# Kernel tuning notes

Measured on AMD Instinct MI355X. Metric: run time of the kernel, lower is better.

## Reference

```python
import jax, jax.numpy as jnp
import numpy as np
from math import sqrt

D_MODEL = 1024
N_HEADS = 16
FFN = 4096
B, N = 2, 2048
EPS = 1e-5


def _layernorm(x, g, b):
    mu = jnp.mean(x, -1, keepdims=True)
    var = jnp.mean((x - mu) ** 2, -1, keepdims=True)
    return (x - mu) * jax.lax.rsqrt(var + EPS) * g + b


def setup_inputs() -> dict:
    key = jax.random.key(0)
    ks = jax.random.split(key, 12)
    s = 1.0 / sqrt(D_MODEL)
    sf = 1.0 / sqrt(FFN)
    inp = {
        "tgt": jax.random.normal(ks[0], (B, N, D_MODEL), jnp.float32),
        # True = masked. Causal: query i may attend to keys j <= i.
        "tgt_mask": jnp.triu(jnp.ones((N, N), jnp.bool_), k=1),
        "tgt_key_pad_mask": jnp.zeros((B, N), jnp.bool_),
        "Wq": jax.random.uniform(ks[1], (D_MODEL, D_MODEL), jnp.float32, -s, s),
        "Wk": jax.random.uniform(ks[2], (D_MODEL, D_MODEL), jnp.float32, -s, s),
        "Wv": jax.random.uniform(ks[3], (D_MODEL, D_MODEL), jnp.float32, -s, s),
        "Wo": jax.random.uniform(ks[4], (D_MODEL, D_MODEL), jnp.float32, -s, s),
        "bo": jax.random.uniform(ks[5], (D_MODEL,), jnp.float32, -s, s),
        "W1": jax.random.uniform(ks[6], (FFN, D_MODEL), jnp.float32, -s, s),
        "b1": jax.random.uniform(ks[7], (FFN,), jnp.float32, -s, s),
        "W2": jax.random.uniform(ks[8], (D_MODEL, FFN), jnp.float32, -sf, sf),
        "b2": jax.random.uniform(ks[9], (D_MODEL,), jnp.float32, -sf, sf),
        "g1": jnp.ones((D_MODEL,), jnp.float32),
        "beta1": jnp.zeros((D_MODEL,), jnp.float32),
        "g2": jnp.ones((D_MODEL,), jnp.float32),
        "beta2": jnp.zeros((D_MODEL,), jnp.float32),
    }
    return inp


def _mha(x, tgt_mask, pad_mask, Wq, Wk, Wv, Wo, bo):
    b, n, d = x.shape
    dk = d // N_HEADS
    q = (x @ Wq.T).reshape(b, n, N_HEADS, dk).transpose(0, 2, 1, 3)  # bhnd
    k = (x @ Wk.T).reshape(b, n, N_HEADS, dk).transpose(0, 2, 1, 3)
    v = (x @ Wv.T).reshape(b, n, N_HEADS, dk).transpose(0, 2, 1, 3)
    scores = jnp.einsum("bhqd,bhkd->bhqk", q, k) / sqrt(dk)
    mask = tgt_mask[None, None, :, :] | pad_mask[:, None, None, :]
    scores = jnp.where(mask, -jnp.inf, scores)
    att = jax.nn.softmax(scores, axis=-1)
    out = jnp.einsum("bhqk,bhkd->bhqd", att, v).transpose(0, 2, 1, 3).reshape(b, n, d)
    return out @ Wo.T + bo


def reference(tgt, tgt_mask, tgt_key_pad_mask, Wq, Wk, Wv, Wo, bo,
              W1, b1, W2, b2, g1, beta1, g2, beta2):
    # PostNorm logic (pre_norm=False), dropout=0 (eval)
    h = _mha(tgt, tgt_mask, tgt_key_pad_mask, Wq, Wk, Wv, Wo, bo)
    x = _layernorm(tgt + h, g1, beta1)
    m = jax.nn.gelu(x @ W1.T + b1, approximate=True) @ W2.T + b2
    return _layernorm(x + m, g2, beta2)
```

## Files before the change

### kernel.cpp

```cpp
#include <hip/hip_runtime.h>


#define DEV __device__ __forceinline__

typedef __attribute__((ext_vector_type(4)))  float f32x4;
typedef __attribute__((ext_vector_type(16))) float f32x16;
typedef __attribute__((ext_vector_type(8)))  short s16x8;

static constexpr int Bb   = 2;
static constexpr int NN   = 2048;
static constexpr int DM   = 1024;
static constexpr int HH   = 16;
static constexpr int DK   = 64;
static constexpr int FF   = 4096;
static constexpr int ROWS = Bb * NN;

#define AS1(p) ((const __attribute__((address_space(1))) void*)(p))
#define AS3(p) ((__attribute__((address_space(3))) void*)(p))

DEV unsigned short f2bf(float f) {
  unsigned u = __float_as_uint(f);
  u += 0x7fff + ((u >> 16) & 1);
  return (unsigned short)(u >> 16);
}
DEV float fexp2(float x) {
  float r;
  asm("v_exp_f32 %0, %1" : "=v"(r) : "v"(x));
  return r;
}
DEV unsigned cvtpk(float lo, float hi) {
  unsigned r;
  asm("v_cvt_pk_bf16_f32 %0, %1, %2" : "=v"(r) : "v"(lo), "v"(hi));
  return r;
}

__global__ __launch_bounds__(256) void k_cast7(
    const float* __restrict__ tgt, const float* __restrict__ Wq,
    const float* __restrict__ Wk, const float* __restrict__ Wv,
    const float* __restrict__ Wo, const float* __restrict__ W1,
    const float* __restrict__ W2,
    ushort* __restrict__ xb, ushort* __restrict__ wqb,
    ushort* __restrict__ w1b, ushort* __restrict__ w2b) {
  const int i = blockIdx.x * 256 + threadIdx.x;
  constexpr int S0 = 1048576;
  constexpr int S1 = 262144;
  const float4* src;
  ushort* dstp;
  if (i < S0)               { src = (const float4*)tgt + i;            dstp = xb  + (size_t)i * 4; }
  else if (i < S0 + S1)     { src = (const float4*)Wq + (i - S0);      dstp = wqb + (size_t)(i - S0) * 4; }
  else if (i < S0 + 2 * S1) { src = (const float4*)Wk + (i - S0 - S1); dstp = wqb + (size_t)(i - S0) * 4; }
  else if (i < S0 + 3 * S1) { src = (const float4*)Wv + (i - S0 - 2 * S1); dstp = wqb + (size_t)(i - S0) * 4; }
  else if (i < S0 + 4 * S1) { src = (const float4*)Wo + (i - S0 - 3 * S1); dstp = wqb + (size_t)(i - S0) * 4; }
  else if (i < 3 * S0)      { src = (const float4*)W1 + (i - 2 * S0);  dstp = w1b + (size_t)(i - 2 * S0) * 4; }
  else                      { src = (const float4*)W2 + (i - 3 * S0);  dstp = w2b + (size_t)(i - 3 * S0) * 4; }
  float4 v = *src;
  ushort4 o;
  o.x = f2bf(v.x); o.y = f2bf(v.y); o.z = f2bf(v.z); o.w = f2bf(v.w);
  *reinterpret_cast<ushort4*>(dstp) = o;
}

template <int EPI, int BN, bool QKV, int SPLITK>
__global__ __launch_bounds__(256) void k_gemm(
    const ushort* __restrict__ A, const ushort* __restrict__ Bt,
    const float* __restrict__ bias, const float* __restrict__ resid,
    ushort* __restrict__ Cb, float* __restrict__ Cf,
    int K, int nbx) {
  __shared__ ushort As[3][128][32];
  __shared__ ushort Bs[3][BN][32];

  const int t = threadIdx.x;
  const int lane = t & 63, w = t >> 6;
  const int lr = lane & 15, lg = lane >> 4;
  const int lrow = lane >> 2, lc8 = (lane & 3) * 8;

  const int nwg = gridDim.x;
  const int bid = blockIdx.x;
  const int q8 = nwg >> 3, r8 = nwg & 7;
  const int xcd = bid & 7, lin = bid >> 3;
  int wg = (xcd < r8 ? xcd * (q8 + 1) : r8 * (q8 + 1) + (xcd - r8) * q8) + lin;
  int kc = 0;
  if constexpr (SPLITK == 2) { kc = wg & 1; wg >>= 1; }
  const int band = wg / (4 * nbx);
  const int inn  = wg % (4 * nbx);
  const int by = band * 4 + (inn & 3);
  const int bx = inn >> 2;

  const int bRow = by * 128;
  const int bCol = bx * BN;
  const int Kc = K / SPLITK;
  const int kofs = kc * Kc;
  const int nk = Kc / 32;

  constexpr int NW = BN / 32;
  const int wRow = (w >> 1) * 64, wCol = (w & 1) * (BN / 2);

  const f32x4 zero = {0.f, 0.f, 0.f, 0.f};
  f32x4 acc[4][NW];
#pragma unroll
  for (int m = 0; m < 4; ++m)
#pragma unroll
    for (int n = 0; n < NW; ++n) acc[m][n] = zero;

  auto stage = [&](int buf, int tile) {
    const int kb = kofs + tile * 32;
#pragma unroll
    for (int i = 0; i < 2; ++i) {
      int rr = w * 32 + i * 16;
      __builtin_amdgcn_global_load_lds(
          AS1(A + (size_t)(bRow + rr + lrow) * K + kb + lc8),
          AS3(&As[buf][rr][0]), 16, 0, 0);
    }
#pragma unroll
    for (int i = 0; i < BN / 64; ++i) {
      int rr = w * (BN / 4) + i * 16;
      __builtin_amdgcn_global_load_lds(
          AS1(Bt + (size_t)(bCol + rr + lrow) * K + kb + lc8),
          AS3(&Bs[buf][rr][0]), 16, 0, 0);
    }
  };

  stage(0, 0);
  stage(1, 1);
  for (int tt = 0; tt < nk; ++tt) {
    const int cur = tt % 3;
    if (tt + 2 < nk) {
      stage((tt + 2) % 3, tt + 2);
      if constexpr (BN == 128) asm volatile("s_waitcnt vmcnt(8)" ::: "memory");
      else                     asm volatile("s_waitcnt vmcnt(6)" ::: "memory");
    } else if (tt + 1 < nk) {
      if constexpr (BN == 128) asm volatile("s_waitcnt vmcnt(4)" ::: "memory");
      else                     asm volatile("s_waitcnt vmcnt(3)" ::: "memory");
    } else {
      asm volatile("s_waitcnt vmcnt(0)" ::: "memory");
    }
    __builtin_amdgcn_s_barrier();
    __builtin_amdgcn_sched_barrier(0);

    s16x8 af[4], bfr[NW];
#pragma unroll
    for (int m = 0; m < 4; ++m)
      af[m] = *reinterpret_cast<const s16x8*>(&As[cur][wRow + m * 16 + lr][lg * 8]);
#pragma unroll
    for (int n = 0; n < NW; ++n)
      bfr[n] = *reinterpret_cast<const s16x8*>(&Bs[cur][wCol + n * 16 + lr][lg * 8]);
#pragma unroll
    for (int m = 0; m < 4; ++m)
#pragma unroll
      for (int n = 0; n < NW; ++n)
        acc[m][n] = __builtin_amdgcn_mfma_f32_16x16x32_bf16(af[m], bfr[n], acc[m][n], 0, 0, 0);

    asm volatile("s_waitcnt lgkmcnt(0)" ::: "memory");
    __builtin_amdgcn_s_barrier();
    __builtin_amdgcn_sched_barrier(0);
  }

  ushort* CbOut = Cb;
  int colBase = bCol, Ncols = nbx * BN, third = 0;
  if (QKV) {
    third = bCol >> 10;
    CbOut = Cb + (size_t)third * ROWS * DM;
    colBase = bCol & 1023;
    Ncols = DM;
  }
#pragma unroll
  for (int m = 0; m < 4; ++m) {
    int gr = bRow + wRow + m * 16 + lg * 4;
#pragma unroll
    for (int n = 0; n < NW; ++n) {
      int gc = colBase + wCol + n * 16 + lr;
      float bv = (EPI == 1 || EPI == 2) ? bias[gc] : 0.0f;
#pragma unroll
      for (int r = 0; r < 4; ++r) {
        int nr = gr + r;
        float v = acc[m][n][r] + bv;
        if (EPI == 3) {
          Cf[((size_t)kc * ROWS + nr) * Ncols + gc] = v;
        } else if (EPI == 2) {
          size_t idx = (size_t)nr * Ncols + gc;
          Cf[idx] = v + resid[idx];
        } else if (EPI == 1) {
          size_t idx = (size_t)nr * Ncols + gc;
          float u = v + 0.044715f * v * v * v;
          float g = v / (1.0f + __expf(-1.5957691216057308f * u));
          CbOut[idx] = f2bf(g);
        } else {
          int gcs = gc;
          if (QKV && third == 1)
            gcs = (gc & ~63) | ((gc ^ ((nr & 7) << 3)) & 63);
          CbOut[(size_t)nr * Ncols + gcs] = f2bf(v);
        }
      }
    }
  }
}

__global__ __launch_bounds__(256) void k_vt(const ushort* __restrict__ V,
                                            ushort* __restrict__ vT) {
  __shared__ ushort Ls[64][72];
  const int t = threadIdx.x;
  const int n0 = blockIdx.x * 64;
  const int bh = blockIdx.y;
  const int b = bh >> 4, h = bh & 15;
  const int n = t >> 2;
#pragma unroll
  for (int half = 0; half < 2; ++half) {
    int c8 = ((t & 3) + half * 4) * 8;
    int4 v = *reinterpret_cast<const int4*>(
        V + ((size_t)(b * NN + n0 + n)) * DM + h * DK + c8);
    *reinterpret_cast<int4*>(&Ls[n][c8]) = v;
  }
  __syncthreads();
  const int d = t >> 2;
#pragma unroll
  for (int half = 0; half < 2; ++half) {
    int c = (t & 3) + half * 4;
    ushort tmp[8];
#pragma unroll
    for (int j = 0; j < 8; ++j) tmp[j] = Ls[c * 8 + j][d];
    size_t out = ((size_t)bh * DK + d) * NN + n0 + ((c ^ (d & 7)) * 8);
    *reinterpret_cast<int4*>(vT + out) = *reinterpret_cast<const int4*>(tmp);
  }
}

template <int WB, int RED>
__global__ __launch_bounds__(256) void k_ln(const float* __restrict__ in,
                                            const float* __restrict__ p0,
                                            const float* __restrict__ p1,
                                            const float* __restrict__ pb,
                                            const float* __restrict__ g,
                                            const float* __restrict__ bta,
                                            float* __restrict__ outf,
                                            ushort* __restrict__ outb) {
  const int row = blockIdx.x;
  const int t = threadIdx.x;
  float4 v = reinterpret_cast<const float4*>(in + (size_t)row * DM)[t];
  if (RED) {
    float4 a = reinterpret_cast<const float4*>(p0 + (size_t)row * DM)[t];
    float4 b = reinterpret_cast<const float4*>(p1 + (size_t)row * DM)[t];
    float4 c = reinterpret_cast<const float4*>(pb)[t];
    v.x += a.x + b.x + c.x;
    v.y += a.y + b.y + c.y;
    v.z += a.z + b.z + c.z;
    v.w += a.w + b.w + c.w;
  }
  float s1 = v.x + v.y + v.z + v.w;
  float s2 = v.x * v.x + v.y * v.y + v.z * v.z + v.w * v.w;
#pragma unroll
  for (int m = 32; m; m >>= 1) {
    s1 += __shfl_xor(s1, m, 64);
    s2 += __shfl_xor(s2, m, 64);
  }
  __shared__ float red[2][4];
  if ((t & 63) == 0) { red[0][t >> 6] = s1; red[1][t >> 6] = s2; }
  __syncthreads();
  s1 = red[0][0] + red[0][1] + red[0][2] + red[0][3];
  s2 = red[1][0] + red[1][1] + red[1][2] + red[1][3];
  const float mu = s1 * (1.0f / DM);
  const float var = s2 * (1.0f / DM) - mu * mu;
  const float rstd = rsqrtf(var + 1e-5f);
  float4 gv = reinterpret_cast<const float4*>(g)[t];
  float4 bv = reinterpret_cast<const float4*>(bta)[t];
  float4 o;
  o.x = (v.x - mu) * rstd * gv.x + bv.x;
  o.y = (v.y - mu) * rstd * gv.y + bv.y;
  o.z = (v.z - mu) * rstd * gv.z + bv.z;
  o.w = (v.w - mu) * rstd * gv.w + bv.w;
  reinterpret_cast<float4*>(outf + (size_t)row * DM)[t] = o;
  if (WB) {
    ushort4 ob;
    ob.x = f2bf(o.x); ob.y = f2bf(o.y); ob.z = f2bf(o.z); ob.w = f2bf(o.w);
    reinterpret_cast<ushort4*>(outb + (size_t)row * DM)[t] = ob;
  }
}

static __device__ const unsigned char SCHED24[24][2] = {
  {15,0},{15,1},{7,2},
  {14,0},{14,1},{13,0},{13,1},{6,2},
  {12,0},{12,1},{11,0},{11,1},{5,2},
  {10,0},{10,1},{9,0},{9,1},{4,2},
  {8,0},{8,1},{3,2},{2,2},{1,2},{0,2}};

__global__ __launch_bounds__(256) void k_attn(const ushort* __restrict__ Q,
                                              const ushort* __restrict__ Kb,
                                              const ushort* __restrict__ vT,
                                              ushort* __restrict__ O,
                                              float* __restrict__ Op,
                                              float* __restrict__ ml) {
  __shared__ ushort Ks[2][64 * 64];
  __shared__ ushort Vs[2][64 * 64];

  const int t = threadIdx.x;
  const int bid = blockIdx.x;
  const int xcd = bid & 7, j = bid >> 3;
  const int head = j / 24, e = j % 24;
  const int qi = SCHED24[e][0], sv = SCHED24[e][1];
  const int bh = xcd * 4 + head;
  const int kt0 = (sv == 1) ? (qi + 1) : 0;
  const int kt1 = (sv == 0) ? (qi + 1) : (2 * qi + 2);

  const int lane = t & 63, wid = t >> 6;
  const int l31 = lane & 31, hi = lane >> 5;
  const int q0w = qi * 128 + wid * 32;
  const size_t qbase = ((size_t)(bh >> 4) * NN) * DM + (bh & 15) * DK;
  const size_t vbase = (size_t)bh * DK * NN;

  const float C = 0.18033688011112043f;

  s16x8 qf[4];
#pragma unroll
  for (int c = 0; c < 4; ++c)
    qf[c] = *reinterpret_cast<const s16x8*>(Q + qbase + (size_t)(q0w + l31) * DM + c * 16 + hi * 8);

  float mrun = -1e30f, lrun = 0.f, negcm = 1e30f;
  f32x16 accO[2];
#pragma unroll
  for (int dt = 0; dt < 2; ++dt)
#pragma unroll
    for (int r = 0; r < 16; ++r) accO[dt][r] = 0.f;

  auto stage = [&](int buf, int kt) {
    const int kk = kt * 64;
#pragma unroll
    for (int i = 0; i < 2; ++i) {
      int row0 = wid * 16 + i * 8;
      __builtin_amdgcn_global_load_lds(
          AS1(Kb + qbase + (size_t)(kk + row0 + (lane >> 3)) * DM + (lane & 7) * 8),
          AS3(&Ks[buf][row0 * 64]), 16, 0, 0);
      __builtin_amdgcn_global_load_lds(
          AS1(vT + vbase + (size_t)(row0 + (lane >> 3)) * NN + kk + (lane & 7) * 8),
          AS3(&Vs[buf][row0 * 64]), 16, 0, 0);
    }
  };

  stage(0, kt0);
  for (int kt = kt0, li = 0; kt < kt1; ++kt, ++li) {
    const int cur = li & 1;
    const int kk = kt * 64;
    __syncthreads();
    if (kt + 1 < kt1) stage(cur ^ 1, kt + 1);

    if (kk <= q0w + 31) {
      const char* KsB = (const char*)Ks[cur];
      const char* VsB = (const char*)Vs[cur];
      const bool diag = (kk + 64 > q0w);
      const int nsub = (kk + 32 <= q0w + 31) ? 2 : 1;

      f32x16 st[2];
      __builtin_amdgcn_s_setprio(1);
#pragma unroll
      for (int sub = 0; sub < 2; ++sub) {
        if (sub >= nsub) break;
#pragma unroll
        for (int r = 0; r < 16; ++r) st[sub][r] = 0.f;
        const int row = sub * 32 + l31;
        const int swz = (row & 7) << 4;
#pragma unroll
        for (int c = 0; c < 4; ++c) {
          s16x8 kf = *reinterpret_cast<const s16x8*>(KsB + row * 128 + ((c * 32 + hi * 16) ^ swz));
          st[sub] = __builtin_amdgcn_mfma_f32_32x32x16_bf16(kf, qf[c], st[sub], 0, 0, 0);
        }
      }
      __builtin_amdgcn_s_setprio(0);

      const int q = q0w + l31;
      float p[32];
#pragma unroll
      for (int sub = 0; sub < 2; ++sub) {
        if (sub >= nsub) break;
#pragma unroll
        for (int r = 0; r < 16; ++r) {
          float v = st[sub][r];
          if (diag) {
            int kl = sub * 32 + (r & 3) + 8 * (r >> 2) + 4 * hi;
            if (kk + kl > q) v = -1e30f;
          }
          p[sub * 16 + r] = v;
        }
      }
      float a[16];
#pragma unroll
      for (int i = 0; i < 16; ++i) a[i] = (nsub == 2) ? fmaxf(p[i], p[i + 16]) : p[i];
#pragma unroll
      for (int s = 8; s; s >>= 1)
#pragma unroll
        for (int i = 0; i < 8; ++i) if (i < s) a[i] = fmaxf(a[i], a[i + s]);
      float rm = fmaxf(a[0], __shfl_xor(a[0], 32, 64));

      if (__any(rm > mrun)) {
        const float mn = fmaxf(mrun, rm);
        const float alpha = fexp2(C * (mrun - mn));
        mrun = mn;
        negcm = -C * mn;
        lrun *= alpha;
#pragma unroll
        for (int dt = 0; dt < 2; ++dt) accO[dt] *= alpha;
      }

#pragma unroll
      for (int sub = 0; sub < 2; ++sub) {
        if (sub >= nsub) break;
#pragma unroll
        for (int i = 0; i < 16; ++i)
          p[sub * 16 + i] = fexp2(fmaf(p[sub * 16 + i], C, negcm));
      }
#pragma unroll
      for (int i = 0; i < 16; ++i) a[i] = (nsub == 2) ? (p[i] + p[i + 16]) : p[i];
#pragma unroll
      for (int s = 8; s; s >>= 1)
#pragma unroll
        for (int i = 0; i < 8; ++i) if (i < s) a[i] += a[i + s];
      lrun += a[0] + __shfl_xor(a[0], 32, 64);

      s16x8 pf[4];
#pragma unroll
      for (int sub = 0; sub < 2; ++sub) {
        if (sub >= nsub) break;
#pragma unroll
        for (int hf = 0; hf < 2; ++hf) {
          const float* pp = &p[sub * 16 + hf * 8];
          unsigned X0 = cvtpk(pp[0], pp[1]);
          unsigned X1 = cvtpk(pp[2], pp[3]);
          unsigned Y0 = cvtpk(pp[4], pp[5]);
          unsigned Y1 = cvtpk(pp[6], pp[7]);
          asm volatile("v_permlane32_swap_b32 %0, %1" : "+v"(X0), "+v"(Y0));
          asm volatile("v_permlane32_swap_b32 %0, %1" : "+v"(X1), "+v"(Y1));
          union { unsigned u[4]; s16x8 v; } uu;
          uu.u[0] = X0; uu.u[1] = X1; uu.u[2] = Y0; uu.u[3] = Y1;
          pf[sub * 2 + hf] = uu.v;
        }
      }

      __builtin_amdgcn_s_setprio(1);
#pragma unroll
      for (int dt = 0; dt < 2; ++dt) {
        const int d = dt * 32 + l31;
        const int vswz = (d & 7) << 4;
#pragma unroll
        for (int kc = 0; kc < 4; ++kc) {
          if (kc >= nsub * 2) break;
          s16x8 vf = *reinterpret_cast<const s16x8*>(VsB + d * 128 + ((kc * 32 + hi * 16) ^ vswz));
          accO[dt] = __builtin_amdgcn_mfma_f32_32x32x16_bf16(vf, pf[kc], accO[dt], 0, 0, 0);
        }
      }
      __builtin_amdgcn_s_setprio(0);
    }
  }

  if (sv == 2) {
    const int q = q0w + l31;
    const float inv = 1.0f / lrun;
#pragma unroll
    for (int dt = 0; dt < 2; ++dt)
#pragma unroll
      for (int rg = 0; rg < 4; ++rg) {
        int d0 = 8 * rg + 4 * hi + 32 * dt;
        ushort4 ov;
        ov.x = f2bf(accO[dt][rg * 4 + 0] * inv);
        ov.y = f2bf(accO[dt][rg * 4 + 1] * inv);
        ov.z = f2bf(accO[dt][rg * 4 + 2] * inv);
        ov.w = f2bf(accO[dt][rg * 4 + 3] * inv);
        *reinterpret_cast<ushort4*>(O + qbase + (size_t)q * DM + d0) = ov;
      }
  } else {
    const int pidx = (bh * 8 + (qi - 8)) * 2 + sv;
    float* op = Op + (size_t)pidx * (128 * 64);
    const int row = wid * 32 + l31;
#pragma unroll
    for (int dt = 0; dt < 2; ++dt)
#pragma unroll
      for (int rg = 0; rg < 4; ++rg) {
        int d0 = 8 * rg + 4 * hi + 32 * dt;
        f32x4 v4 = { accO[dt][rg * 4 + 0], accO[dt][rg * 4 + 1],
                     accO[dt][rg * 4 + 2], accO[dt][rg * 4 + 3] };
        *reinterpret_cast<f32x4*>(op + (size_t)row * 64 + d0) = v4;
      }
    if (hi == 0) {
      ml[(size_t)pidx * 256 + row * 2 + 0] = mrun;
      ml[(size_t)pidx * 256 + row * 2 + 1] = lrun;
    }
  }
}

__global__ __launch_bounds__(256) void k_amerge(const float* __restrict__ Op,
                                                const float* __restrict__ ml,
                                                ushort* __restrict__ O) {
  const int bh = blockIdx.x >> 3, qq = blockIdx.x & 7;
  const int t = threadIdx.x;
  const int row = t >> 1, dh = (t & 1) * 32;
  const float C = 0.18033688011112043f;

  const int p0 = (bh * 8 + qq) * 2;
  const float m0 = ml[(size_t)p0 * 256 + row * 2 + 0];
  const float l0 = ml[(size_t)p0 * 256 + row * 2 + 1];
  const float m1 = ml[(size_t)(p0 + 1) * 256 + row * 2 + 0];
  const float l1 = ml[(size_t)(p0 + 1) * 256 + row * 2 + 1];
  const float M = fmaxf(m0, m1);
  const float s0 = fexp2(C * (m0 - M));
  const float s1 = fexp2(C * (m1 - M));
  const float inv = 1.0f / (l0 * s0 + l1 * s1);

  const float* o0 = Op + (size_t)p0 * (128 * 64) + (size_t)row * 64 + dh;
  const float* o1 = o0 + 128 * 64;
  const int b = bh >> 4, h = bh & 15;
  const int n = (qq + 8) * 128 + row;
  ushort* dst = O + ((size_t)(b * NN + n)) * DM + h * DK + dh;
#pragma unroll
  for (int i = 0; i < 8; ++i) {
    float4 a = reinterpret_cast<const float4*>(o0)[i];
    float4 c = reinterpret_cast<const float4*>(o1)[i];
    ushort4 ov;
    ov.x = f2bf((a.x * s0 + c.x * s1) * inv);
    ov.y = f2bf((a.y * s0 + c.y * s1) * inv);
    ov.z = f2bf((a.z * s0 + c.z * s1) * inv);
    ov.w = f2bf((a.w * s0 + c.w * s1) * inv);
    reinterpret_cast<ushort4*>(dst)[i] = ov;
  }
}

extern "C" void kernel_launch(void* const* d_in, const int* in_sizes, int n_in,
                              void* d_out, int out_size, void* d_ws, size_t ws_size,
                              hipStream_t stream) {
  const float* tgt = (const float*)d_in[0];
  const float* Wq  = (const float*)d_in[3];
  const float* Wk  = (const float*)d_in[4];
  const float* Wv  = (const float*)d_in[5];
  const float* Wo  = (const float*)d_in[6];
  const float* bo  = (const float*)d_in[7];
  const float* W1  = (const float*)d_in[8];
  const float* b1  = (const float*)d_in[9];
  const float* W2  = (const float*)d_in[10];
  const float* b2  = (const float*)d_in[11];
  const float* g1  = (const float*)d_in[12];
  const float* be1 = (const float*)d_in[13];
  const float* g2  = (const float*)d_in[14];
  const float* be2 = (const float*)d_in[15];

  char* ws = (char*)d_ws;
  size_t off = 0;
  auto alloc = [&](size_t bytes) {
    void* p = ws + off;
    off += (bytes + 255) & ~(size_t)255;
    return p;
  };
  ushort* xb   = (ushort*)alloc((size_t)ROWS * DM * 2);
  ushort* wqb  = (ushort*)alloc((size_t)DM * DM * 2);
  ushort* wkb  = (ushort*)alloc((size_t)DM * DM * 2);
  ushort* wvb  = (ushort*)alloc((size_t)DM * DM * 2);
  ushort* wob  = (ushort*)alloc((size_t)DM * DM * 2);
  ushort* w1b  = (ushort*)alloc((size_t)FF * DM * 2);
  ushort* w2b  = (ushort*)alloc((size_t)DM * FF * 2);
  ushort* qbuf = (ushort*)alloc((size_t)ROWS * DM * 2);
  ushort* kbuf = (ushort*)alloc((size_t)ROWS * DM * 2);
  ushort* vbuf = (ushort*)alloc((size_t)ROWS * DM * 2);
  ushort* vtb  = (ushort*)alloc((size_t)ROWS * DM * 2);
  ushort* atnb = (ushort*)alloc((size_t)ROWS * DM * 2);
  float*  h1   = (float*)alloc((size_t)ROWS * DM * 4);
  float*  x1f  = (float*)alloc((size_t)ROWS * DM * 4);
  ushort* x1b  = (ushort*)alloc((size_t)ROWS * DM * 2);
  ushort* t1b  = (ushort*)alloc((size_t)ROWS * FF * 2);
  float*  Opb  = (float*)alloc((size_t)512 * 128 * 64 * 4);
  float*  mlb  = (float*)alloc((size_t)512 * 256 * 4);
  float*  pp   = (float*)qbuf;
  (void)ws_size; (void)in_sizes; (void)n_in; (void)out_size;
  (void)wkb; (void)wvb; (void)kbuf;

  dim3 blk(256);
  k_cast7<<<dim3(16384), blk, 0, stream>>>(tgt, Wq, Wk, Wv, Wo, W1, W2,
                                           xb, wqb, w1b, w2b);

  k_gemm<0, 128, true, 1><<<dim3(24 * 32), blk, 0, stream>>>(
      xb, wqb, nullptr, nullptr, qbuf, nullptr, DM, 24);

  k_vt<<<dim3(NN / 64, Bb * HH), blk, 0, stream>>>(vbuf, vtb);

  k_attn<<<dim3(768), blk, 0, stream>>>(qbuf, kbuf, vtb, atnb, Opb, mlb);
  k_amerge<<<dim3(256), blk, 0, stream>>>(Opb, mlb, atnb);

  k_gemm<2, 64, false, 1><<<dim3(16 * 32), blk, 0, stream>>>(
      atnb, wob, bo, tgt, nullptr, h1, DM, 16);
  k_ln<1, 0><<<dim3(ROWS), blk, 0, stream>>>(h1, nullptr, nullptr, nullptr,
                                             g1, be1, x1f, x1b);

  k_gemm<1, 128, false, 1><<<dim3(32 * 32), blk, 0, stream>>>(
      x1b, w1b, b1, nullptr, t1b, nullptr, DM, 32);
  k_gemm<3, 64, false, 2><<<dim3(2 * 16 * 32), blk, 0, stream>>>(
      t1b, w2b, nullptr, nullptr, nullptr, pp, FF, 16);
  k_ln<0, 1><<<dim3(ROWS), blk, 0, stream>>>(x1f, pp, pp + (size_t)ROWS * DM, b2,
                                             g2, be2, (float*)d_out, nullptr);
}
```

Baseline: 272.2 us.

## Load attention K/V fragments directly from global into registers, dropping LDS staging

The attention kernel no longer stages K and V tiles through shared memory with global_load_lds and block barriers. Each wave now loads its MFMA operand fragments straight from global memory into registers, double-buffering K fragments across iterations and capping the tile loop at the wave's causal limit. The XOR swizzles on K and vT written by the QKV GEMM epilogue and the transpose kernel are removed to match. This removes barrier synchronisation and LDS traffic, but each wave re-reads K/V that its four waves used to share, which adds global/L2 traffic and register pressure.

```diff
diff --git a/kernel.cpp b/kernel.cpp
--- a/kernel.cpp
+++ b/kernel.cpp
@@ -155,10 +155,9 @@
   }
 
   ushort* CbOut = Cb;
-  int colBase = bCol, Ncols = nbx * BN, third = 0;
+  int colBase = bCol, Ncols = nbx * BN;
   if (QKV) {
-    third = bCol >> 10;
-    CbOut = Cb + (size_t)third * ROWS * DM;
+    CbOut = Cb + (size_t)(bCol >> 10) * ROWS * DM;
     colBase = bCol & 1023;
     Ncols = DM;
   }
@@ -184,10 +183,7 @@
           float g = v / (1.0f + __expf(-1.5957691216057308f * u));
           CbOut[idx] = f2bf(g);
         } else {
-          int gcs = gc;
-          if (QKV && third == 1)
-            gcs = (gc & ~63) | ((gc ^ ((nr & 7) << 3)) & 63);
-          CbOut[(size_t)nr * Ncols + gcs] = f2bf(v);
+          CbOut[(size_t)nr * Ncols + gc] = f2bf(v);
         }
       }
     }
@@ -217,7 +213,7 @@
     ushort tmp[8];
 #pragma unroll
     for (int j = 0; j < 8; ++j) tmp[j] = Ls[c * 8 + j][d];
-    size_t out = ((size_t)bh * DK + d) * NN + n0 + ((c ^ (d & 7)) * 8);
+    size_t out = ((size_t)bh * DK + d) * NN + n0 + c * 8;
     *reinterpret_cast<int4*>(vT + out) = *reinterpret_cast<const int4*>(tmp);
   }
 }
@@ -286,9 +282,6 @@
                                               ushort* __restrict__ O,
                                               float* __restrict__ Op,
                                               float* __restrict__ ml) {
-  __shared__ ushort Ks[2][64 * 64];
-  __shared__ ushort Vs[2][64 * 64];
-
   const int t = threadIdx.x;
   const int bid = blockIdx.x;
   const int xcd = bid & 7, j = bid >> 3;
@@ -303,8 +296,10 @@
   const int q0w = qi * 128 + wid * 32;
   const size_t qbase = ((size_t)(bh >> 4) * NN) * DM + (bh & 15) * DK;
   const size_t vbase = (size_t)bh * DK * NN;
-
   const float C = 0.18033688011112043f;
+
+  const int ktcap = ((q0w + 31) >> 6) + 1;
+  const int ktend = (kt1 < ktcap) ? kt1 : ktcap;
 
   s16x8 qf[4];
 #pragma unroll
@@ -318,132 +313,138 @@
 #pragma unroll
     for (int r = 0; r < 16; ++r) accO[dt][r] = 0.f;
 
-  auto stage = [&](int buf, int kt) {
+  const ushort* kRow = Kb + qbase + (size_t)l31 * DM + hi * 8;
+  const ushort* vRow = vT + vbase + (size_t)l31 * NN + hi * 8;
+
+  s16x8 kfA[8], kfB[8], vf[8];
+
+  auto loadK = [&](s16x8* kf, int kt) {
+#pragma unroll
+    for (int sub = 0; sub < 2; ++sub)
+#pragma unroll
+      for (int c = 0; c < 4; ++c)
+        kf[sub * 4 + c] = *reinterpret_cast<const s16x8*>(
+            kRow + (size_t)(kt * 64 + sub * 32) * DM + c * 16);
+  };
+  auto loadV = [&](int kt) {
+#pragma unroll
+    for (int dt = 0; dt < 2; ++dt)
+#pragma unroll
+      for (int kc = 0; kc < 4; ++kc)
+        vf[dt * 4 + kc] = *reinterpret_cast<const s16x8*>(
+            vRow + (size_t)(dt * 32) * NN + kt * 64 + kc * 16);
+  };
+
+  auto tilecomp = [&](const s16x8* kf, int kt) {
     const int kk = kt * 64;
-#pragma unroll
-    for (int i = 0; i < 2; ++i) {
-      int row0 = wid * 16 + i * 8;
-      __builtin_amdgcn_global_load_lds(
-          AS1(Kb + qbase + (size_t)(kk + row0 + (lane >> 3)) * DM + (lane & 7) * 8),
-          AS3(&Ks[buf][row0 * 64]), 16, 0, 0);
-      __builtin_amdgcn_global_load_lds(
-          AS1(vT + vbase + (size_t)(row0 + (lane >> 3)) * NN + kk + (lane & 7) * 8),
-          AS3(&Vs[buf][row0 * 64]), 16, 0, 0);
-    }
+    const bool diag = (kk + 64 > q0w);
+    const int nsub = (kk + 32 <= q0w + 31) ? 2 : 1;
+
+    f32x16 st[2];
+    __builtin_amdgcn_s_setprio(1);
+#pragma unroll
+    for (int sub = 0; sub < 2; ++sub) {
+      if (sub >= nsub) break;
+#pragma unroll
+      for (int r = 0; r < 16; ++r) st[sub][r] = 0.f;
+#pragma unroll
+      for (int c = 0; c < 4; ++c)
+        st[sub] = __builtin_amdgcn_mfma_f32_32x32x16_bf16(kf[sub * 4 + c], qf[c], st[sub], 0, 0, 0);
+    }
+    __builtin_amdgcn_s_setprio(0);
+
+    const int q = q0w + l31;
+    float p[32];
+#pragma unroll
+    for (int sub = 0; sub < 2; ++sub) {
+      if (sub >= nsub) break;
+#pragma unroll
+      for (int r = 0; r < 16; ++r) {
+        float v = st[sub][r];
+        if (diag) {
+          int kl = sub * 32 + (r & 3) + 8 * (r >> 2) + 4 * hi;
+          if (kk + kl > q) v = -1e30f;
+        }
+        p[sub * 16 + r] = v;
+      }
+    }
+    float a[16];
+#pragma unroll
+    for (int i = 0; i < 16; ++i) a[i] = (nsub == 2) ? fmaxf(p[i], p[i + 16]) : p[i];
+#pragma unroll
+    for (int s = 8; s; s >>= 1)
+#pragma unroll
+      for (int i = 0; i < 8; ++i) if (i < s) a[i] = fmaxf(a[i], a[i + s]);
+    float rm = fmaxf(a[0], __shfl_xor(a[0], 32, 64));
+
+    if (__any(rm > mrun)) {
+      const float mn = fmaxf(mrun, rm);
+      const float alpha = fexp2(C * (mrun - mn));
+      mrun = mn;
+      negcm = -C * mn;
+      lrun *= alpha;
+#pragma unroll
+      for (int dt = 0; dt < 2; ++dt) accO[dt] *= alpha;
+    }
+
+#pragma unroll
+    for (int sub = 0; sub < 2; ++sub) {
+      if (sub >= nsub) break;
+#pragma unroll
+      for (int i = 0; i < 16; ++i)
+        p[sub * 16 + i] = fexp2(fmaf(p[sub * 16 + i], C, negcm));
+    }
+#pragma unroll
+    for (int i = 0; i < 16; ++i) a[i] = (nsub == 2) ? (p[i] + p[i + 16]) : p[i];
+#pragma unroll
+    for (int s = 8; s; s >>= 1)
+#pragma unroll
+      for (int i = 0; i < 8; ++i) if (i < s) a[i] += a[i + s];
+    lrun += a[0] + __shfl_xor(a[0], 32, 64);
+
+    s16x8 pf[4];
+#pragma unroll
+    for (int sub = 0; sub < 2; ++sub) {
+      if (sub >= nsub) break;
+#pragma unroll
+      for (int hf = 0; hf < 2; ++hf) {
+        const float* pp = &p[sub * 16 + hf * 8];
+        unsigned X0 = cvtpk(pp[0], pp[1]);
+        unsigned X1 = cvtpk(pp[2], pp[3]);
+        unsigned Y0 = cvtpk(pp[4], pp[5]);
+        unsigned Y1 = cvtpk(pp[6], pp[7]);
+        asm volatile("v_permlane32_swap_b32 %0, %1" : "+v"(X0), "+v"(Y0));
+        asm volatile("v_permlane32_swap_b32 %0, %1" : "+v"(X1), "+v"(Y1));
+        union { unsigned u[4]; s16x8 v; } uu;
+        uu.u[0] = X0; uu.u[1] = X1; uu.u[2] = Y0; uu.u[3] = Y1;
+        pf[sub * 2 + hf] = uu.v;
+      }
+    }
+
+    __builtin_amdgcn_s_setprio(1);
+#pragma unroll
+    for (int dt = 0; dt < 2; ++dt) {
+#pragma unroll
+      for (int kc = 0; kc < 4; ++kc) {
+        if (kc >= nsub * 2) break;
+        accO[dt] = __builtin_amdgcn_mfma_f32_32x32x16_bf16(vf[dt * 4 + kc], pf[kc], accO[dt], 0, 0, 0);
+      }
+    }
+    __builtin_amdgcn_s_setprio(0);
   };
 
-  stage(0, kt0);
-  for (int kt = kt0, li = 0; kt < kt1; ++kt, ++li) {
-    const int cur = li & 1;
-    const int kk = kt * 64;
-    __syncthreads();
-    if (kt + 1 < kt1) stage(cur ^ 1, kt + 1);
-
-    if (kk <= q0w + 31) {
-      const char* KsB = (const char*)Ks[cur];
-      const char* VsB = (const char*)Vs[cur];
-      const bool diag = (kk + 64 > q0w);
-      const int nsub = (kk + 32 <= q0w + 31) ? 2 : 1;
-
-      f32x16 st[2];
-      __builtin_amdgcn_s_setprio(1);
-#pragma unroll
-      for (int sub = 0; sub < 2; ++sub) {
-        if (sub >= nsub) break;
-#pragma unroll
-        for (int r = 0; r < 16; ++r) st[sub][r] = 0.f;
-        const int row = sub * 32 + l31;
-        const int swz = (row & 7) << 4;
-#pragma unroll
-        for (int c = 0; c < 4; ++c) {
-          s16x8 kf = *reinterpret_cast<const s16x8*>(KsB + row * 128 + ((c * 32 + hi * 16) ^ swz));
-          st[sub] = __builtin_amdgcn_mfma_f32_32x32x16_bf16(kf, qf[c], st[sub], 0, 0, 0);
-        }
-      }
-      __builtin_amdgcn_s_setprio(0);
-
-      const int q = q0w + l31;
-      float p[32];
-#pragma unroll
-      for (int sub = 0; sub < 2; ++sub) {
-        if (sub >= nsub) break;
-#pragma unroll
-        for (int r = 0; r < 16; ++r) {
-          float v = st[sub][r];
-          if (diag) {
-            int kl = sub * 32 + (r & 3) + 8 * (r >> 2) + 4 * hi;
-            if (kk + kl > q) v = -1e30f;
-          }
-          p[sub * 16 + r] = v;
-        }
-      }
-      float a[16];
-#pragma unroll
-      for (int i = 0; i < 16; ++i) a[i] = (nsub == 2) ? fmaxf(p[i], p[i + 16]) : p[i];
-#pragma unroll
-      for (int s = 8; s; s >>= 1)
-#pragma unroll
-        for (int i = 0; i < 8; ++i) if (i < s) a[i] = fmaxf(a[i], a[i + s]);
-      float rm = fmaxf(a[0], __shfl_xor(a[0], 32, 64));
-
-      if (__any(rm > mrun)) {
-        const float mn = fmaxf(mrun, rm);
-        const float alpha = fexp2(C * (mrun - mn));
-        mrun = mn;
-        negcm = -C * mn;
-        lrun *= alpha;
-#pragma unroll
-        for (int dt = 0; dt < 2; ++dt) accO[dt] *= alpha;
-      }
-
-#pragma unroll
-      for (int sub = 0; sub < 2; ++sub) {
-        if (sub >= nsub) break;
-#pragma unroll
-        for (int i = 0; i < 16; ++i)
-          p[sub * 16 + i] = fexp2(fmaf(p[sub * 16 + i], C, negcm));
-      }
-#pragma unroll
-      for (int i = 0; i < 16; ++i) a[i] = (nsub == 2) ? (p[i] + p[i + 16]) : p[i];
-#pragma unroll
-      for (int s = 8; s; s >>= 1)
-#pragma unroll
-        for (int i = 0; i < 8; ++i) if (i < s) a[i] += a[i + s];
-      lrun += a[0] + __shfl_xor(a[0], 32, 64);
-
-      s16x8 pf[4];
-#pragma unroll
-      for (int sub = 0; sub < 2; ++sub) {
-        if (sub >= nsub) break;
-#pragma unroll
-        for (int hf = 0; hf < 2; ++hf) {
-          const float* pp = &p[sub * 16 + hf * 8];
-          unsigned X0 = cvtpk(pp[0], pp[1]);
-          unsigned X1 = cvtpk(pp[2], pp[3]);
-          unsigned Y0 = cvtpk(pp[4], pp[5]);
-          unsigned Y1 = cvtpk(pp[6], pp[7]);
-          asm volatile("v_permlane32_swap_b32 %0, %1" : "+v"(X0), "+v"(Y0));
-          asm volatile("v_permlane32_swap_b32 %0, %1" : "+v"(X1), "+v"(Y1));
-          union { unsigned u[4]; s16x8 v; } uu;
-          uu.u[0] = X0; uu.u[1] = X1; uu.u[2] = Y0; uu.u[3] = Y1;
-          pf[sub * 2 + hf] = uu.v;
-        }
-      }
-
-      __builtin_amdgcn_s_setprio(1);
-#pragma unroll
-      for (int dt = 0; dt < 2; ++dt) {
-        const int d = dt * 32 + l31;
-        const int vswz = (d & 7) << 4;
-#pragma unroll
-        for (int kc = 0; kc < 4; ++kc) {
-          if (kc >= nsub * 2) break;
-          s16x8 vf = *reinterpret_cast<const s16x8*>(VsB + d * 128 + ((kc * 32 + hi * 16) ^ vswz));
-          accO[dt] = __builtin_amdgcn_mfma_f32_32x32x16_bf16(vf, pf[kc], accO[dt], 0, 0, 0);
-        }
-      }
-      __builtin_amdgcn_s_setprio(0);
-    }
+  int kt = kt0;
+  if (kt < ktend) loadK(kfA, kt);
+  while (kt < ktend) {
+    loadV(kt);
+    if (kt + 1 < ktend) loadK(kfB, kt + 1);
+    tilecomp(kfA, kt);
+    ++kt;
+    if (kt >= ktend) break;
+    loadV(kt);
+    if (kt + 1 < ktend) loadK(kfA, kt + 1);
+    tilecomp(kfB, kt);
+    ++kt;
   }
 
   if (sv == 2) {
```

Result: slower. 291.9 us (+7.2%).

## Split causal attention KV into up to four segments with generalized merge

Applied to the files above, without the earlier changes.

Replaces the fixed 24-entry split-KV schedule with a 40-entry schedule where long query tiles are split into up to four KV segments (for qi>=4), and generalizes the merge kernel to combine a variable number of partials. The partial output buffer now aliases the h1 activation buffer instead of a dedicated allocation. This aims to balance per-block work across CUs, at the cost of more partial traffic and merge work, and relies on the aliased region (spilling past h1) being dead at that point.

```diff
diff --git a/kernel.cpp b/kernel.cpp
--- a/kernel.cpp
+++ b/kernel.cpp
@@ -273,12 +273,13 @@
   }
 }
 
-static __device__ const unsigned char SCHED24[24][2] = {
-  {15,0},{15,1},{7,2},
-  {14,0},{14,1},{13,0},{13,1},{6,2},
-  {12,0},{12,1},{11,0},{11,1},{5,2},
-  {10,0},{10,1},{9,0},{9,1},{4,2},
-  {8,0},{8,1},{3,2},{2,2},{1,2},{0,2}};
+static __device__ const unsigned char SCHED40[40][2] = {
+  {15,0},{15,1},{15,2},{15,3}, {14,0},{14,1},{14,2},{14,3},
+  {13,0},{13,1},{13,2},{13,3}, {12,0},{12,1},{12,2},{12,3},
+  {11,0},{11,1},{11,2}, {10,0},{10,1},{10,2},
+  {9,0},{9,1},{9,2}, {8,0},{8,1},{8,2},
+  {7,0},{7,1}, {6,0},{6,1}, {5,0},{5,1}, {4,0},{4,1},
+  {3,0},{2,0},{1,0},{0,0}};
 
 __global__ __launch_bounds__(256) void k_attn(const ushort* __restrict__ Q,
                                               const ushort* __restrict__ Kb,
@@ -292,11 +293,14 @@
   const int t = threadIdx.x;
   const int bid = blockIdx.x;
   const int xcd = bid & 7, j = bid >> 3;
-  const int head = j / 24, e = j % 24;
-  const int qi = SCHED24[e][0], sv = SCHED24[e][1];
+  const int head = j & 3, e = j >> 2;
+  const int qi = SCHED40[e][0], seg = SCHED40[e][1];
   const int bh = xcd * 4 + head;
-  const int kt0 = (sv == 1) ? (qi + 1) : 0;
-  const int kt1 = (sv == 0) ? (qi + 1) : (2 * qi + 2);
+  const int ntiles = 2 * qi + 2;
+  const int nseg = (2 * qi + 9) >> 3;
+  const int tb = ntiles / nseg, rem = ntiles % nseg;
+  const int kt0 = seg * tb + (seg < rem ? seg : rem);
+  const int kt1 = kt0 + tb + (seg < rem ? 1 : 0);
 
   const int lane = t & 63, wid = t >> 6;
   const int l31 = lane & 31, hi = lane >> 5;
@@ -446,7 +450,7 @@
     }
   }
 
-  if (sv == 2) {
+  if (nseg == 1) {
     const int q = q0w + l31;
     const float inv = 1.0f / lrun;
 #pragma unroll
@@ -462,7 +466,7 @@
         *reinterpret_cast<ushort4*>(O + qbase + (size_t)q * DM + d0) = ov;
       }
   } else {
-    const int pidx = (bh * 8 + (qi - 8)) * 2 + sv;
+    const int pidx = (bh * 12 + (qi - 4)) * 4 + seg;
     float* op = Op + (size_t)pidx * (128 * 64);
     const int row = wid * 32 + l31;
 #pragma unroll
@@ -484,35 +488,49 @@
 __global__ __launch_bounds__(256) void k_amerge(const float* __restrict__ Op,
                                                 const float* __restrict__ ml,
                                                 ushort* __restrict__ O) {
-  const int bh = blockIdx.x >> 3, qq = blockIdx.x & 7;
+  const int bid = blockIdx.x;
+  const int bh = bid / 12, qq = bid % 12;
+  const int qi = qq + 4;
+  const int nseg = (2 * qi + 9) >> 3;
   const int t = threadIdx.x;
   const int row = t >> 1, dh = (t & 1) * 32;
   const float C = 0.18033688011112043f;
-
-  const int p0 = (bh * 8 + qq) * 2;
-  const float m0 = ml[(size_t)p0 * 256 + row * 2 + 0];
-  const float l0 = ml[(size_t)p0 * 256 + row * 2 + 1];
-  const float m1 = ml[(size_t)(p0 + 1) * 256 + row * 2 + 0];
-  const float l1 = ml[(size_t)(p0 + 1) * 256 + row * 2 + 1];
-  const float M = fmaxf(m0, m1);
-  const float s0 = fexp2(C * (m0 - M));
-  const float s1 = fexp2(C * (m1 - M));
-  const float inv = 1.0f / (l0 * s0 + l1 * s1);
-
-  const float* o0 = Op + (size_t)p0 * (128 * 64) + (size_t)row * 64 + dh;
-  const float* o1 = o0 + 128 * 64;
+  const int pbase = (bh * 12 + qq) * 4;
+
+  float M = -1e30f;
+  for (int s = 0; s < nseg; ++s)
+    M = fmaxf(M, ml[(size_t)(pbase + s) * 256 + row * 2 + 0]);
+  float wsum = 0.f;
+  for (int s = 0; s < nseg; ++s) {
+    float ms = ml[(size_t)(pbase + s) * 256 + row * 2 + 0];
+    float ls = ml[(size_t)(pbase + s) * 256 + row * 2 + 1];
+    wsum += ls * fexp2(C * (ms - M));
+  }
+  const float inv = 1.0f / wsum;
+
+  f32x4 acc[8];
+#pragma unroll
+  for (int i = 0; i < 8; ++i) acc[i] = (f32x4){0.f, 0.f, 0.f, 0.f};
+  for (int s = 0; s < nseg; ++s) {
+    float ws = fexp2(C * (ml[(size_t)(pbase + s) * 256 + row * 2 + 0] - M));
+    const float* os = Op + (size_t)(pbase + s) * (128 * 64) + (size_t)row * 64 + dh;
+#pragma unroll
+    for (int i = 0; i < 8; ++i) {
+      f32x4 v = reinterpret_cast<const f32x4*>(os)[i];
+      acc[i] += v * ws;
+    }
+  }
+
   const int b = bh >> 4, h = bh & 15;
-  const int n = (qq + 8) * 128 + row;
+  const int n = qi * 128 + row;
   ushort* dst = O + ((size_t)(b * NN + n)) * DM + h * DK + dh;
 #pragma unroll
   for (int i = 0; i < 8; ++i) {
-    float4 a = reinterpret_cast<const float4*>(o0)[i];
-    float4 c = reinterpret_cast<const float4*>(o1)[i];
     ushort4 ov;
-    ov.x = f2bf((a.x * s0 + c.x * s1) * inv);
-    ov.y = f2bf((a.y * s0 + c.y * s1) * inv);
-    ov.z = f2bf((a.z * s0 + c.z * s1) * inv);
-    ov.w = f2bf((a.w * s0 + c.w * s1) * inv);
+    ov.x = f2bf(acc[i][0] * inv);
+    ov.y = f2bf(acc[i][1] * inv);
+    ov.z = f2bf(acc[i][2] * inv);
+    ov.w = f2bf(acc[i][3] * inv);
     reinterpret_cast<ushort4*>(dst)[i] = ov;
   }
 }
@@ -558,8 +576,8 @@
   float*  x1f  = (float*)alloc((size_t)ROWS * DM * 4);
   ushort* x1b  = (ushort*)alloc((size_t)ROWS * DM * 2);
   ushort* t1b  = (ushort*)alloc((size_t)ROWS * FF * 2);
-  float*  Opb  = (float*)alloc((size_t)512 * 128 * 64 * 4);
-  float*  mlb  = (float*)alloc((size_t)512 * 256 * 4);
+  float*  mlb  = (float*)alloc((size_t)1536 * 256 * 4);
+  float*  Opb  = h1;
   float*  pp   = (float*)qbuf;
   (void)ws_size; (void)in_sizes; (void)n_in; (void)out_size;
   (void)wkb; (void)wvb; (void)kbuf;
@@ -573,8 +591,8 @@
 
   k_vt<<<dim3(NN / 64, Bb * HH), blk, 0, stream>>>(vbuf, vtb);
 
-  k_attn<<<dim3(768), blk, 0, stream>>>(qbuf, kbuf, vtb, atnb, Opb, mlb);
-  k_amerge<<<dim3(256), blk, 0, stream>>>(Opb, mlb, atnb);
+  k_attn<<<dim3(1280), blk, 0, stream>>>(qbuf, kbuf, vtb, atnb, Opb, mlb);
+  k_amerge<<<dim3(384), blk, 0, stream>>>(Opb, mlb, atnb);
 
   k_gemm<2, 64, false, 1><<<dim3(16 * 32), blk, 0, stream>>>(
       atnb, wob, bo, tgt, nullptr, h1, DM, 16);
```

After: 269.3 us. Within noise of the previous version (-1.0%).
